# Kernel tuning notes

Hardware: AMD Instinct MI355X
Metric: run time of the kernel (lower is better)

## Reference

```python
import jax, jax.numpy as jnp
import numpy as np

D_MODEL = 1024
NUM_HEADS = 16
D_K = D_MODEL // NUM_HEADS


def setup_inputs() -> dict:
    key = jax.random.key(0)
    ks = jax.random.split(key, 11)
    B, S = 4, 2048
    s = 1.0 / np.sqrt(D_MODEL)
    return {
        "q": jax.random.normal(ks[0], (B, S, D_MODEL), jnp.float32),
        "k": jax.random.normal(ks[1], (B, S, D_MODEL), jnp.float32),
        "v": jax.random.normal(ks[2], (B, S, D_MODEL), jnp.float32),
        "w_q": jax.random.normal(ks[3], (D_MODEL, D_MODEL), jnp.float32) * s,
        "b_q": jnp.zeros((D_MODEL,), jnp.float32),
        "w_k": jax.random.normal(ks[4], (D_MODEL, D_MODEL), jnp.float32) * s,
        "b_k": jnp.zeros((D_MODEL,), jnp.float32),
        "w_v": jax.random.normal(ks[5], (D_MODEL, D_MODEL), jnp.float32) * s,
        "b_v": jnp.zeros((D_MODEL,), jnp.float32),
        "w_o": jax.random.normal(ks[6], (D_MODEL, D_MODEL), jnp.float32) * s,
        "b_o": jnp.zeros((D_MODEL,), jnp.float32),
    }


def reference(q, k, v, w_q, b_q, w_k, b_k, w_v, b_v, w_o, b_o):
    B, S, _ = q.shape
    # projections; torch Linear computes x @ W.T + b
    def proj(x, w, b):
        y = x @ w.T + b
        return y.reshape(B, -1, NUM_HEADS, D_K).transpose(0, 2, 1, 3)  # (B,H,S,d_k)

    qh, kh, vh = proj(q, w_q, b_q), proj(k, w_k, b_k), proj(v, w_v, b_v)
    scores = jnp.einsum("bhqd,bhkd->bhqk", qh, kh) / jnp.sqrt(jnp.float32(D_K))
    attn_weights = jax.nn.softmax(scores, axis=-1)
    x = jnp.einsum("bhqk,bhkd->bhqd", attn_weights, vh)
    x = x.transpose(0, 2, 1, 3).reshape(B, -1, D_MODEL)
    out = x @ w_o.T + b_o
    return out, attn_weights
```

## Files before the change

kernel.cpp:

```cpp
#include <hip/hip_runtime.h>
#include <math.h>

#define S_LEN 2048
#define DM 1024
#define NH 16
#define DK 64

typedef __attribute__((ext_vector_type(8))) short short8;
typedef __attribute__((ext_vector_type(4))) short short4v;
typedef __attribute__((ext_vector_type(4))) float f32x4;

__device__ __forceinline__ short f2bf(float f) {
  unsigned u = __builtin_bit_cast(unsigned, f);
  u = (u + 0x7FFFu + ((u >> 16) & 1u)) >> 16;
  return (short)u;
}

__device__ __forceinline__ void gld_lds16(const short* g, short* l) {
  __builtin_amdgcn_global_load_lds(
      (const __attribute__((address_space(1))) unsigned int*)g,
      (__attribute__((address_space(3))) unsigned int*)l, 16, 0, 0);
}

__global__ __launch_bounds__(256) void cvt_bf16(
    const float* __restrict__ s0, const float* __restrict__ s1,
    const float* __restrict__ s2, const float* __restrict__ s3,
    short* __restrict__ d0, short* __restrict__ d1,
    short* __restrict__ d2, short* __restrict__ d3, int n)
{
  const float* s; short* d;
  switch (blockIdx.y) {
    case 0:  s = s0; d = d0; break;
    case 1:  s = s1; d = d1; break;
    case 2:  s = s2; d = d2; break;
    default: s = s3; d = d3; break;
  }
  const int i = (blockIdx.x * 256 + threadIdx.x) * 8;
  if (i < n) {
    const float4 v0 = *(const float4*)&s[i];
    const float4 v1 = *(const float4*)&s[i + 4];
    short8 r = { f2bf(v0.x), f2bf(v0.y), f2bf(v0.z), f2bf(v0.w),
                 f2bf(v1.x), f2bf(v1.y), f2bf(v1.z), f2bf(v1.w) };
    *(short8*)&d[i] = r;
  }
}

__global__ __launch_bounds__(256) void proj3(
    const short* __restrict__ qb, const short* __restrict__ kb, const short* __restrict__ vb,
    const short* __restrict__ wqb, const short* __restrict__ wkb, const short* __restrict__ wvb,
    const float* __restrict__ biq, const float* __restrict__ bik, const float* __restrict__ biv,
    short* __restrict__ qhb, short* __restrict__ khb, short* __restrict__ vtb)
{
  __shared__ short As[128 * 32];
  __shared__ short Bs[128 * 32];
  const int z = blockIdx.z;
  const short* A; const short* B; const float* bias; short* o;
  if (z == 0)      { A = qb; B = wqb; bias = biq; o = qhb; }
  else if (z == 1) { A = kb; B = wkb; bias = bik; o = khb; }
  else             { A = vb; B = wvb; bias = biv; o = vtb; }

  const int tid = threadIdx.x;
  const int lane = tid & 63;
  const int wv = tid >> 6;
  const int grp = lane >> 4, lid = lane & 15;
  const int wr = wv >> 1, wc = wv & 1;
  const int bm = blockIdx.x, bn = blockIdx.y;

  f32x4 acc[4][4] = {};

  const int idx0 = tid, idx1 = 256 + tid;
  const int r0 = idx0 >> 2, c0 = (idx0 & 3) * 8;
  const int r1 = idx1 >> 2, c1 = (idx1 & 3) * 8;
  const short* a0 = &A[(size_t)(bm * 128 + r0) * DM + c0];
  const short* a1 = &A[(size_t)(bm * 128 + r1) * DM + c1];
  const short* b0 = &B[(size_t)(bn * 128 + r0) * DM + c0];
  const short* b1 = &B[(size_t)(bn * 128 + r1) * DM + c1];

  for (int ks = 0; ks < 32; ++ks) {
    __syncthreads();
    gld_lds16(a0 + ks * 32, &As[idx0 * 8]);
    gld_lds16(a1 + ks * 32, &As[idx1 * 8]);
    gld_lds16(b0 + ks * 32, &Bs[idx0 * 8]);
    gld_lds16(b1 + ks * 32, &Bs[idx1 * 8]);
    __syncthreads();
    short8 a[4], b[4];
    #pragma unroll
    for (int m = 0; m < 4; ++m) a[m] = *(const short8*)&As[(wr * 64 + m * 16 + lid) * 32 + grp * 8];
    #pragma unroll
    for (int n = 0; n < 4; ++n) b[n] = *(const short8*)&Bs[(wc * 64 + n * 16 + lid) * 32 + grp * 8];
    #pragma unroll
    for (int m = 0; m < 4; ++m)
      #pragma unroll
      for (int n = 0; n < 4; ++n)
        acc[m][n] = __builtin_amdgcn_mfma_f32_16x16x32_bf16(a[m], b[n], acc[m][n], 0, 0, 0);
  }

  #pragma unroll
  for (int n = 0; n < 4; ++n) {
    const int ng = bn * 128 + wc * 64 + n * 16 + lid;
    const float bvs = bias[ng];
    const int h = ng >> 6, d = ng & 63;
    #pragma unroll
    for (int m = 0; m < 4; ++m) {
      const int mg = bm * 128 + wr * 64 + m * 16 + grp * 4;
      const int bb = mg >> 11, s = mg & 2047;
      if (z < 2) {
        #pragma unroll
        for (int r = 0; r < 4; ++r)
          o[(((size_t)bb * NH + h) * S_LEN + s + r) * DK + d] = f2bf(acc[m][n][r] + bvs);
      } else {
        short4v sv = { f2bf(acc[m][n][0] + bvs), f2bf(acc[m][n][1] + bvs),
                       f2bf(acc[m][n][2] + bvs), f2bf(acc[m][n][3] + bvs) };
        *(short4v*)&o[(((size_t)bb * NH + h) * DK + d) * S_LEN + s] = sv;
      }
    }
  }
}

__global__ __launch_bounds__(256) void gemm_o(
    const short* __restrict__ A, const short* __restrict__ B,
    const float* __restrict__ bias, float* __restrict__ of)
{
  __shared__ short As[128 * 32];
  __shared__ short Bs[128 * 32];
  const int tid = threadIdx.x;
  const int lane = tid & 63;
  const int wv = tid >> 6;
  const int grp = lane >> 4, lid = lane & 15;
  const int wr = wv >> 1, wc = wv & 1;
  const int bm = blockIdx.x, bn = blockIdx.y;

  f32x4 acc[4][4] = {};

  const int idx0 = tid, idx1 = 256 + tid;
  const int r0 = idx0 >> 2, c0 = (idx0 & 3) * 8;
  const int r1 = idx1 >> 2, c1 = (idx1 & 3) * 8;
  const short* a0 = &A[(size_t)(bm * 128 + r0) * DM + c0];
  const short* a1 = &A[(size_t)(bm * 128 + r1) * DM + c1];
  const short* b0 = &B[(size_t)(bn * 128 + r0) * DM + c0];
  const short* b1 = &B[(size_t)(bn * 128 + r1) * DM + c1];

  for (int ks = 0; ks < 32; ++ks) {
    __syncthreads();
    gld_lds16(a0 + ks * 32, &As[idx0 * 8]);
    gld_lds16(a1 + ks * 32, &As[idx1 * 8]);
    gld_lds16(b0 + ks * 32, &Bs[idx0 * 8]);
    gld_lds16(b1 + ks * 32, &Bs[idx1 * 8]);
    __syncthreads();
    short8 a[4], b[4];
    #pragma unroll
    for (int m = 0; m < 4; ++m) a[m] = *(const short8*)&As[(wr * 64 + m * 16 + lid) * 32 + grp * 8];
    #pragma unroll
    for (int n = 0; n < 4; ++n) b[n] = *(const short8*)&Bs[(wc * 64 + n * 16 + lid) * 32 + grp * 8];
    #pragma unroll
    for (int m = 0; m < 4; ++m)
      #pragma unroll
      for (int n = 0; n < 4; ++n)
        acc[m][n] = __builtin_amdgcn_mfma_f32_16x16x32_bf16(a[m], b[n], acc[m][n], 0, 0, 0);
  }

  #pragma unroll
  for (int n = 0; n < 4; ++n) {
    const int ng = bn * 128 + wc * 64 + n * 16 + lid;
    const float bvs = bias[ng];
    #pragma unroll
    for (int m = 0; m < 4; ++m) {
      const int mg = bm * 128 + wr * 64 + m * 16 + grp * 4;
      #pragma unroll
      for (int r = 0; r < 4; ++r)
        __builtin_nontemporal_store(acc[m][n][r] + bvs, &of[(size_t)(mg + r) * DM + ng]);
    }
  }
}

__global__ __launch_bounds__(256) void mha_attn5(
    const short* __restrict__ qh, const short* __restrict__ kh, const short* __restrict__ vt,
    float* __restrict__ attn, short* __restrict__ xb)
{
  __shared__ short Kt[64][72];
  __shared__ short Vt[64][72];
  __shared__ short Ps[4][32][72];

  const int tid = threadIdx.x;
  const int lane = tid & 63, wv = tid >> 6, grp = lane >> 4, lid = lane & 15;

  const int nid = blockIdx.x;
  const int x = nid & 7, jj = nid >> 3;
  const int bh = x + 8 * (jj >> 4);
  const int qt = jj & 15;

  const size_t baseQ = (size_t)bh * S_LEN * DK;
  const size_t baseV = (size_t)bh * DK * S_LEN;
  const float scale = 0.125f;

  const short* Qb = qh + baseQ;
  const short* Kb = kh + baseQ;
  const short* Vb = vt + baseV;

  const int id0 = tid, id1 = tid + 256;
  const int tr0 = id0 >> 3, tc0 = (id0 & 7) * 8;
  const int tr1 = id1 >> 3, tc1 = (id1 & 7) * 8;

  short8 aq[2][2];
  #pragma unroll
  for (int mf = 0; mf < 2; ++mf)
    #pragma unroll
    for (int kf = 0; kf < 2; ++kf)
      aq[mf][kf] = *(const short8*)&Qb[(size_t)(qt * 128 + wv * 32 + mf * 16 + lid) * DK + kf * 32 + grp * 8];

  float lsum[2][4] = {};

  for (int kt = 0; kt < 32; ++kt) {
    const short8 k0 = *(const short8*)&Kb[(size_t)(kt * 64 + tr0) * DK + tc0];
    const short8 k1 = *(const short8*)&Kb[(size_t)(kt * 64 + tr1) * DK + tc1];
    __syncthreads();
    *(short8*)&Kt[tr0][tc0] = k0;
    *(short8*)&Kt[tr1][tc1] = k1;
    __syncthreads();
    f32x4 sacc[2][4] = {};
    __builtin_amdgcn_s_setprio(1);
    #pragma unroll
    for (int kf = 0; kf < 2; ++kf) {
      short8 bk[4];
      #pragma unroll
      for (int nf = 0; nf < 4; ++nf) bk[nf] = *(const short8*)&Kt[nf * 16 + lid][kf * 32 + grp * 8];
      #pragma unroll
      for (int mf = 0; mf < 2; ++mf)
        #pragma unroll
        for (int nf = 0; nf < 4; ++nf)
          sacc[mf][nf] = __builtin_amdgcn_mfma_f32_16x16x32_bf16(aq[mf][kf], bk[nf], sacc[mf][nf], 0, 0, 0);
    }
    __builtin_amdgcn_s_setprio(0);
    #pragma unroll
    for (int mf = 0; mf < 2; ++mf)
      #pragma unroll
      for (int r = 0; r < 4; ++r)
        #pragma unroll
        for (int nf = 0; nf < 4; ++nf)
          lsum[mf][r] += __expf(sacc[mf][nf][r] * scale);
  }

  float rl[2][4];
  #pragma unroll
  for (int mf = 0; mf < 2; ++mf)
    #pragma unroll
    for (int r = 0; r < 4; ++r) {
      float s = lsum[mf][r];
      #pragma unroll
      for (int off = 8; off >= 1; off >>= 1) s += __shfl_xor(s, off, 16);
      rl[mf][r] = 1.f / s;
    }

  f32x4 oacc[2][4] = {};
  float* attnB = attn + ((size_t)bh * S_LEN + qt * 128 + wv * 32) * S_LEN;

  for (int kt = 0; kt < 32; ++kt) {
    const short8 k0 = *(const short8*)&Kb[(size_t)(kt * 64 + tr0) * DK + tc0];
    const short8 k1 = *(const short8*)&Kb[(size_t)(kt * 64 + tr1) * DK + tc1];
    const short8 v0 = *(const short8*)&Vb[(size_t)tr0 * S_LEN + kt * 64 + tc0];
    const short8 v1 = *(const short8*)&Vb[(size_t)tr1 * S_LEN + kt * 64 + tc1];
    __syncthreads();
    *(short8*)&Kt[tr0][tc0] = k0;
    *(short8*)&Kt[tr1][tc1] = k1;
    *(short8*)&Vt[tr0][tc0] = v0;
    *(short8*)&Vt[tr1][tc1] = v1;
    __syncthreads();

    f32x4 sacc[2][4] = {};
    __builtin_amdgcn_s_setprio(1);
    #pragma unroll
    for (int kf = 0; kf < 2; ++kf) {
      short8 bk[4];
      #pragma unroll
      for (int nf = 0; nf < 4; ++nf) bk[nf] = *(const short8*)&Kt[nf * 16 + lid][kf * 32 + grp * 8];
      #pragma unroll
      for (int mf = 0; mf < 2; ++mf)
        #pragma unroll
        for (int nf = 0; nf < 4; ++nf)
          sacc[mf][nf] = __builtin_amdgcn_mfma_f32_16x16x32_bf16(aq[mf][kf], bk[nf], sacc[mf][nf], 0, 0, 0);
    }
    __builtin_amdgcn_s_setprio(0);

    #pragma unroll
    for (int mf = 0; mf < 2; ++mf)
      #pragma unroll
      for (int nf = 0; nf < 4; ++nf)
        #pragma unroll
        for (int r = 0; r < 4; ++r) {
          const float p = __expf(sacc[mf][nf][r] * scale) * rl[mf][r];
          Ps[wv][mf * 16 + grp * 4 + r][nf * 16 + lid] = f2bf(p);
        }

    __builtin_amdgcn_s_setprio(1);
    #pragma unroll
    for (int kf = 0; kf < 2; ++kf) {
      short8 ap[2], bvv[4];
      #pragma unroll
      for (int mf = 0; mf < 2; ++mf) ap[mf] = *(const short8*)&Ps[wv][mf * 16 + lid][kf * 32 + grp * 8];
      #pragma unroll
      for (int nf = 0; nf < 4; ++nf) bvv[nf] = *(const short8*)&Vt[nf * 16 + lid][kf * 32 + grp * 8];
      #pragma unroll
      for (int mf = 0; mf < 2; ++mf)
        #pragma unroll
        for (int nf = 0; nf < 4; ++nf)
          oacc[mf][nf] = __builtin_amdgcn_mfma_f32_16x16x32_bf16(ap[mf], bvv[nf], oacc[mf][nf], 0, 0, 0);
    }
    __builtin_amdgcn_s_setprio(0);

    #pragma unroll
    for (int i = 0; i < 8; ++i) {
      const int qrow = i * 4 + grp;
      const uint2 u = *(const uint2*)&Ps[wv][qrow][lid * 4];
      f32x4 f;
      f[0] = __builtin_bit_cast(float, u.x << 16);
      f[1] = __builtin_bit_cast(float, u.x & 0xffff0000u);
      f[2] = __builtin_bit_cast(float, u.y << 16);
      f[3] = __builtin_bit_cast(float, u.y & 0xffff0000u);
      __builtin_nontemporal_store(f, (f32x4*)&attnB[(size_t)qrow * S_LEN + kt * 64 + lid * 4]);
    }
  }

  const int b = bh >> 4, h = bh & 15;
  #pragma unroll
  for (int mf = 0; mf < 2; ++mf) {
    #pragma unroll
    for (int nf = 0; nf < 4; ++nf) {
      #pragma unroll
      for (int r = 0; r < 4; ++r) {
        const int s = qt * 128 + wv * 32 + mf * 16 + grp * 4 + r;
        const int d = nf * 16 + lid;
        xb[((size_t)b * S_LEN + s) * DM + h * DK + d] = f2bf(oacc[mf][nf][r]);
      }
    }
  }
}

template<int MODE>
__global__ __launch_bounds__(256) void mha_gemm(
    const float* __restrict__ Af, const short* __restrict__ Ab,
    const float* __restrict__ W, const float* __restrict__ bias,
    short* __restrict__ obf, float* __restrict__ of)
{
  __shared__ short As[128][40];
  __shared__ short Bs[128][40];
  const int tid = threadIdx.x;
  const int lane = tid & 63, wv = tid >> 6;
  const int grp = lane >> 4, lid = lane & 15;
  const int wr = wv >> 1, wc = wv & 1;
  const int bm = blockIdx.x, bn = blockIdx.y;

  f32x4 acc[4][4] = {};

  for (int ks = 0; ks < 32; ++ks) {
    __syncthreads();
    if (MODE == 0) {
      #pragma unroll
      for (int i = 0; i < 4; ++i) {
        const int c = tid + 256 * i;
        const int row = c >> 3, kc = c & 7;
        const float4 v = *(const float4*)&Af[(size_t)(bm * 128 + row) * DM + ks * 32 + kc * 4];
        short4v s4 = { f2bf(v.x), f2bf(v.y), f2bf(v.z), f2bf(v.w) };
        *(short4v*)&As[row][kc * 4] = s4;
      }
    } else {
      #pragma unroll
      for (int i = 0; i < 2; ++i) {
        const int c = tid + 256 * i;
        const int row = c >> 2, k8 = (c & 3) * 8;
        *(float4*)&As[row][k8] = *(const float4*)&Ab[(size_t)(bm * 128 + row) * DM + ks * 32 + k8];
      }
    }
    #pragma unroll
    for (int i = 0; i < 4; ++i) {
      const int c = tid + 256 * i;
      const int row = c >> 3, kc = c & 7;
      const float4 v = *(const float4*)&W[(size_t)(bn * 128 + row) * DM + ks * 32 + kc * 4];
      short4v s4 = { f2bf(v.x), f2bf(v.y), f2bf(v.z), f2bf(v.w) };
      *(short4v*)&Bs[row][kc * 4] = s4;
    }
    __syncthreads();
    short8 a[4], b[4];
    #pragma unroll
    for (int m = 0; m < 4; ++m) a[m] = *(const short8*)&As[wr * 64 + m * 16 + lid][grp * 8];
    #pragma unroll
    for (int n = 0; n < 4; ++n) b[n] = *(const short8*)&Bs[wc * 64 + n * 16 + lid][grp * 8];
    #pragma unroll
    for (int m = 0; m < 4; ++m)
      #pragma unroll
      for (int n = 0; n < 4; ++n)
        acc[m][n] = __builtin_amdgcn_mfma_f32_16x16x32_bf16(a[m], b[n], acc[m][n], 0, 0, 0);
  }

  #pragma unroll
  for (int n = 0; n < 4; ++n) {
    const int ng = bn * 128 + wc * 64 + n * 16 + lid;
    const float bvs = bias[ng];
    #pragma unroll
    for (int m = 0; m < 4; ++m) {
      const int mg = bm * 128 + wr * 64 + m * 16 + grp * 4;
      #pragma unroll
      for (int r = 0; r < 4; ++r) {
        const float val = acc[m][n][r] + bvs;
        const int mm = mg + r;
        if (MODE == 0) {
          const int bb = mm >> 11, s = mm & 2047, h = ng >> 6, d = ng & 63;
          obf[(((size_t)bb * NH + h) * S_LEN + s) * DK + d] = f2bf(val);
        } else {
          of[(size_t)mm * DM + ng] = val;
        }
      }
    }
  }
}

__global__ __launch_bounds__(256) void mha_attn_old(
    const short* __restrict__ qh, const short* __restrict__ kh, const short* __restrict__ vh,
    float* __restrict__ attn, short* __restrict__ xb)
{
  __shared__ short QP[128][72];
  __shared__ short Ks[64][72];
  __shared__ short VT[64][72];

  const int tid = threadIdx.x;
  const int lane = tid & 63, wv = tid >> 6, grp = lane >> 4, lid = lane & 15;
  const int qt = blockIdx.x, bh = blockIdx.y;
  const size_t base = (size_t)bh * S_LEN * DK;
  const float scale = 0.125f;

  #pragma unroll
  for (int i = 0; i < 4; ++i) {
    const int c = tid + 256 * i;
    const int row = c >> 3, k8 = (c & 7) * 8;
    *(float4*)&QP[row][k8] = *(const float4*)&qh[base + (size_t)(qt * 128 + row) * DK + k8];
  }
  __syncthreads();
  short8 aq[2][2];
  #pragma unroll
  for (int mf = 0; mf < 2; ++mf)
    #pragma unroll
    for (int kf = 0; kf < 2; ++kf)
      aq[mf][kf] = *(const short8*)&QP[wv * 32 + mf * 16 + lid][kf * 32 + grp * 8];

  float lsum[2][4] = {};

  for (int kt = 0; kt < 32; ++kt) {
    __syncthreads();
    #pragma unroll
    for (int i = 0; i < 2; ++i) {
      const int c = tid + 256 * i;
      const int row = c >> 3, k8 = (c & 7) * 8;
      *(float4*)&Ks[row][k8] = *(const float4*)&kh[base + (size_t)(kt * 64 + row) * DK + k8];
    }
    __syncthreads();
    f32x4 sacc[2][4] = {};
    #pragma unroll
    for (int kf = 0; kf < 2; ++kf) {
      short8 bk[4];
      #pragma unroll
      for (int nf = 0; nf < 4; ++nf) bk[nf] = *(const short8*)&Ks[nf * 16 + lid][kf * 32 + grp * 8];
      #pragma unroll
      for (int mf = 0; mf < 2; ++mf)
        #pragma unroll
        for (int nf = 0; nf < 4; ++nf)
          sacc[mf][nf] = __builtin_amdgcn_mfma_f32_16x16x32_bf16(aq[mf][kf], bk[nf], sacc[mf][nf], 0, 0, 0);
    }
    #pragma unroll
    for (int mf = 0; mf < 2; ++mf)
      #pragma unroll
      for (int r = 0; r < 4; ++r)
        #pragma unroll
        for (int nf = 0; nf < 4; ++nf)
          lsum[mf][r] += __expf(sacc[mf][nf][r] * scale);
  }

  float rl[2][4];
  #pragma unroll
  for (int mf = 0; mf < 2; ++mf)
    #pragma unroll
    for (int r = 0; r < 4; ++r) {
      float s = lsum[mf][r];
      #pragma unroll
      for (int off = 8; off >= 1; off >>= 1) s += __shfl_xor(s, off, 16);
      rl[mf][r] = 1.f / s;
    }

  f32x4 oacc[2][4] = {};

  for (int kt = 0; kt < 32; ++kt) {
    __syncthreads();
    #pragma unroll
    for (int i = 0; i < 2; ++i) {
      const int c = tid + 256 * i;
      const int row = c >> 3, k8 = (c & 7) * 8;
      *(float4*)&Ks[row][k8] = *(const float4*)&kh[base + (size_t)(kt * 64 + row) * DK + k8];
    }
    #pragma unroll
    for (int i = 0; i < 2; ++i) {
      const int key = tid & 63;
      const int d0 = ((tid >> 6) << 3) + i * 32;
      const float4 v = *(const float4*)&vh[base + (size_t)(kt * 64 + key) * DK + d0];
      const short8 sv = __builtin_bit_cast(short8, v);
      #pragma unroll
      for (int jj = 0; jj < 8; ++jj) VT[d0 + jj][key] = sv[jj];
    }
    __syncthreads();
    f32x4 sacc[2][4] = {};
    #pragma unroll
    for (int kf = 0; kf < 2; ++kf) {
      short8 bk[4];
      #pragma unroll
      for (int nf = 0; nf < 4; ++nf) bk[nf] = *(const short8*)&Ks[nf * 16 + lid][kf * 32 + grp * 8];
      #pragma unroll
      for (int mf = 0; mf < 2; ++mf)
        #pragma unroll
        for (int nf = 0; nf < 4; ++nf)
          sacc[mf][nf] = __builtin_amdgcn_mfma_f32_16x16x32_bf16(aq[mf][kf], bk[nf], sacc[mf][nf], 0, 0, 0);
    }
    #pragma unroll
    for (int mf = 0; mf < 2; ++mf) {
      #pragma unroll
      for (int nf = 0; nf < 4; ++nf) {
        #pragma unroll
        for (int r = 0; r < 4; ++r) {
          const float p = __expf(sacc[mf][nf][r] * scale) * rl[mf][r];
          const int qr = wv * 32 + mf * 16 + grp * 4 + r;
          const int kc = kt * 64 + nf * 16 + lid;
          attn[((size_t)bh * S_LEN + qt * 128 + qr) * S_LEN + kc] = p;
          QP[wv * 32 + (qr & 31)][nf * 16 + lid] = f2bf(p);
        }
      }
    }
    #pragma unroll
    for (int kf = 0; kf < 2; ++kf) {
      short8 ap[2], bvv[4];
      #pragma unroll
      for (int mf = 0; mf < 2; ++mf) ap[mf] = *(const short8*)&QP[wv * 32 + mf * 16 + lid][kf * 32 + grp * 8];
      #pragma unroll
      for (int nf = 0; nf < 4; ++nf) bvv[nf] = *(const short8*)&VT[nf * 16 + lid][kf * 32 + grp * 8];
      #pragma unroll
      for (int mf = 0; mf < 2; ++mf)
        #pragma unroll
        for (int nf = 0; nf < 4; ++nf)
          oacc[mf][nf] = __builtin_amdgcn_mfma_f32_16x16x32_bf16(ap[mf], bvv[nf], oacc[mf][nf], 0, 0, 0);
    }
  }

  const int b = bh >> 4, h = bh & 15;
  #pragma unroll
  for (int mf = 0; mf < 2; ++mf) {
    #pragma unroll
    for (int nf = 0; nf < 4; ++nf) {
      #pragma unroll
      for (int r = 0; r < 4; ++r) {
        const int s = qt * 128 + wv * 32 + mf * 16 + grp * 4 + r;
        const int d = nf * 16 + lid;
        xb[((size_t)b * S_LEN + s) * DM + h * DK + d] = f2bf(oacc[mf][nf][r]);
      }
    }
  }
}

extern "C" void kernel_launch(void* const* d_in, const int* in_sizes, int n_in,
                              void* d_out, int out_size, void* d_ws, size_t ws_size,
                              hipStream_t stream) {
  const float* q  = (const float*)d_in[0];
  const float* k  = (const float*)d_in[1];
  const float* v  = (const float*)d_in[2];
  const float* wq = (const float*)d_in[3];
  const float* bq = (const float*)d_in[4];
  const float* wk = (const float*)d_in[5];
  const float* bk = (const float*)d_in[6];
  const float* wv = (const float*)d_in[7];
  const float* bv = (const float*)d_in[8];
  const float* wo = (const float*)d_in[9];
  const float* bo = (const float*)d_in[10];

  float* out  = (float*)d_out;
  float* attn = out + (size_t)4 * S_LEN * DM;

  const size_t NTOK = (size_t)4 * S_LEN * DM;
  const size_t NW   = (size_t)DM * DM;
  dim3 blk(256);

  if (ws_size >= 135000000ull) {
    short* qb  = (short*)d_ws;
    short* kb  = qb + NTOK;
    short* vb  = kb + NTOK;
    short* wqb = vb + NTOK;
    short* wkb = wqb + NW;
    short* wvb = wkb + NW;
    short* wob = wvb + NW;
    short* qhb = wob + NW;
    short* khb = qhb + NTOK;
    short* vtb = khb + NTOK;
    short* xb  = vtb + NTOK;

    cvt_bf16<<<dim3(4096, 3), blk, 0, stream>>>(q, k, v, (const float*)nullptr,
                                                qb, kb, vb, (short*)nullptr, (int)NTOK);
    cvt_bf16<<<dim3(512, 4), blk, 0, stream>>>(wq, wk, wv, wo, wqb, wkb, wvb, wob, (int)NW);

    proj3<<<dim3(64, 8, 3), blk, 0, stream>>>(qb, kb, vb, wqb, wkb, wvb, bq, bk, bv,
                                              qhb, khb, vtb);

    mha_attn5<<<dim3(1024), blk, 0, stream>>>(qhb, khb, vtb, attn, xb);

    gemm_o<<<dim3(64, 8), blk, 0, stream>>>(xb, wob, bo, out);
  } else {
    short* qhb = (short*)d_ws;
    short* khb = qhb + NTOK;
    short* vhb = khb + NTOK;
    short* xb  = vhb + NTOK;

    mha_gemm<0><<<dim3(64, 8), blk, 0, stream>>>(q, (const short*)nullptr, wq, bq, qhb, (float*)nullptr);
    mha_gemm<0><<<dim3(64, 8), blk, 0, stream>>>(k, (const short*)nullptr, wk, bk, khb, (float*)nullptr);
    mha_gemm<0><<<dim3(64, 8), blk, 0, stream>>>(v, (const short*)nullptr, wv, bv, vhb, (float*)nullptr);
    mha_attn_old<<<dim3(16, 64), blk, 0, stream>>>(qhb, khb, vhb, attn, xb);
    mha_gemm<1><<<dim3(64, 8), blk, 0, stream>>>((const float*)nullptr, xb, wo, bo, (short*)nullptr, out);
  }
}
```

Before: 409.6 us.

## Halve attention block size and register-prefetch K/V tiles

The attention kernel now uses 128-thread blocks covering 64 query rows each, launched as 2048 blocks instead of 1024. K and V tiles are prefetched into registers one iteration ahead. The first pass ping-pongs K between two LDS buffers (reusing the Ps region), which removes one barrier per iteration. This aims to hide global load latency and raise occupancy, at the cost of reloading K/V twice as often per head and more registers per thread.

```diff
diff --git a/kernel.cpp b/kernel.cpp
--- a/kernel.cpp
+++ b/kernel.cpp
@@ -173,21 +173,21 @@
   }
 }
 
-__global__ __launch_bounds__(256) void mha_attn5(
+__global__ __launch_bounds__(128) void mha_attn6(
     const short* __restrict__ qh, const short* __restrict__ kh, const short* __restrict__ vt,
     float* __restrict__ attn, short* __restrict__ xb)
 {
   __shared__ short Kt[64][72];
   __shared__ short Vt[64][72];
-  __shared__ short Ps[4][32][72];
+  __shared__ short Ps[2][32][72];
 
   const int tid = threadIdx.x;
   const int lane = tid & 63, wv = tid >> 6, grp = lane >> 4, lid = lane & 15;
 
   const int nid = blockIdx.x;
   const int x = nid & 7, jj = nid >> 3;
-  const int bh = x + 8 * (jj >> 4);
-  const int qt = jj & 15;
+  const int bh = x + 8 * (jj >> 5);
+  const int qt = jj & 31;
 
   const size_t baseQ = (size_t)bh * S_LEN * DK;
   const size_t baseV = (size_t)bh * DK * S_LEN;
@@ -197,25 +197,34 @@
   const short* Kb = kh + baseQ;
   const short* Vb = vt + baseV;
 
-  const int id0 = tid, id1 = tid + 256;
-  const int tr0 = id0 >> 3, tc0 = (id0 & 7) * 8;
-  const int tr1 = id1 >> 3, tc1 = (id1 & 7) * 8;
+  int tr[4], tc[4];
+  #pragma unroll
+  for (int i = 0; i < 4; ++i) {
+    const int id = tid + 128 * i;
+    tr[i] = id >> 3; tc[i] = (id & 7) * 8;
+  }
 
   short8 aq[2][2];
   #pragma unroll
   for (int mf = 0; mf < 2; ++mf)
     #pragma unroll
     for (int kf = 0; kf < 2; ++kf)
-      aq[mf][kf] = *(const short8*)&Qb[(size_t)(qt * 128 + wv * 32 + mf * 16 + lid) * DK + kf * 32 + grp * 8];
+      aq[mf][kf] = *(const short8*)&Qb[(size_t)(qt * 64 + wv * 32 + mf * 16 + lid) * DK + kf * 32 + grp * 8];
 
   float lsum[2][4] = {};
 
+  short8 kr[4];
+  #pragma unroll
+  for (int i = 0; i < 4; ++i) kr[i] = *(const short8*)&Kb[(size_t)tr[i] * DK + tc[i]];
   for (int kt = 0; kt < 32; ++kt) {
-    const short8 k0 = *(const short8*)&Kb[(size_t)(kt * 64 + tr0) * DK + tc0];
-    const short8 k1 = *(const short8*)&Kb[(size_t)(kt * 64 + tr1) * DK + tc1];
-    __syncthreads();
-    *(short8*)&Kt[tr0][tc0] = k0;
-    *(short8*)&Kt[tr1][tc1] = k1;
+    short* buf = (kt & 1) ? &Ps[0][0][0] : &Kt[0][0];
+    #pragma unroll
+    for (int i = 0; i < 4; ++i) *(short8*)&buf[tr[i] * 72 + tc[i]] = kr[i];
+    if (kt < 31) {
+      #pragma unroll
+      for (int i = 0; i < 4; ++i)
+        kr[i] = *(const short8*)&Kb[(size_t)((kt + 1) * 64 + tr[i]) * DK + tc[i]];
+    }
     __syncthreads();
     f32x4 sacc[2][4] = {};
     __builtin_amdgcn_s_setprio(1);
@@ -223,7 +232,7 @@
     for (int kf = 0; kf < 2; ++kf) {
       short8 bk[4];
       #pragma unroll
-      for (int nf = 0; nf < 4; ++nf) bk[nf] = *(const short8*)&Kt[nf * 16 + lid][kf * 32 + grp * 8];
+      for (int nf = 0; nf < 4; ++nf) bk[nf] = *(const short8*)&buf[(nf * 16 + lid) * 72 + kf * 32 + grp * 8];
       #pragma unroll
       for (int mf = 0; mf < 2; ++mf)
         #pragma unroll
@@ -252,18 +261,28 @@
     }
 
   f32x4 oacc[2][4] = {};
-  float* attnB = attn + ((size_t)bh * S_LEN + qt * 128 + wv * 32) * S_LEN;
-
+  float* attnB = attn + ((size_t)bh * S_LEN + qt * 64 + wv * 32) * S_LEN;
+
+  short8 vr[4];
+  #pragma unroll
+  for (int i = 0; i < 4; ++i) {
+    kr[i] = *(const short8*)&Kb[(size_t)tr[i] * DK + tc[i]];
+    vr[i] = *(const short8*)&Vb[(size_t)tr[i] * S_LEN + tc[i]];
+  }
   for (int kt = 0; kt < 32; ++kt) {
-    const short8 k0 = *(const short8*)&Kb[(size_t)(kt * 64 + tr0) * DK + tc0];
-    const short8 k1 = *(const short8*)&Kb[(size_t)(kt * 64 + tr1) * DK + tc1];
-    const short8 v0 = *(const short8*)&Vb[(size_t)tr0 * S_LEN + kt * 64 + tc0];
-    const short8 v1 = *(const short8*)&Vb[(size_t)tr1 * S_LEN + kt * 64 + tc1];
-    __syncthreads();
-    *(short8*)&Kt[tr0][tc0] = k0;
-    *(short8*)&Kt[tr1][tc1] = k1;
-    *(short8*)&Vt[tr0][tc0] = v0;
-    *(short8*)&Vt[tr1][tc1] = v1;
+    __syncthreads();
+    #pragma unroll
+    for (int i = 0; i < 4; ++i) {
+      *(short8*)&Kt[tr[i]][tc[i]] = kr[i];
+      *(short8*)&Vt[tr[i]][tc[i]] = vr[i];
+    }
+    if (kt < 31) {
+      #pragma unroll
+      for (int i = 0; i < 4; ++i) {
+        kr[i] = *(const short8*)&Kb[(size_t)((kt + 1) * 64 + tr[i]) * DK + tc[i]];
+        vr[i] = *(const short8*)&Vb[(size_t)tr[i] * S_LEN + (kt + 1) * 64 + tc[i]];
+      }
+    }
     __syncthreads();
 
     f32x4 sacc[2][4] = {};
@@ -327,7 +346,7 @@
     for (int nf = 0; nf < 4; ++nf) {
       #pragma unroll
       for (int r = 0; r < 4; ++r) {
-        const int s = qt * 128 + wv * 32 + mf * 16 + grp * 4 + r;
+        const int s = qt * 64 + wv * 32 + mf * 16 + grp * 4 + r;
         const int d = nf * 16 + lid;
         xb[((size_t)b * S_LEN + s) * DM + h * DK + d] = f2bf(oacc[mf][nf][r]);
       }
@@ -602,7 +621,7 @@
     proj3<<<dim3(64, 8, 3), blk, 0, stream>>>(qb, kb, vb, wqb, wkb, wvb, bq, bk, bv,
                                               qhb, khb, vtb);
 
-    mha_attn5<<<dim3(1024), blk, 0, stream>>>(qhb, khb, vtb, attn, xb);
+    mha_attn6<<<dim3(2048), dim3(128), 0, stream>>>(qhb, khb, vtb, attn, xb);
 
     gemm_o<<<dim3(64, 8), blk, 0, stream>>>(xb, wob, bo, out);
   } else {
```

Result: faster. 397.2 us (-3.0%).
